# Kernel optimization log

Hardware: AMD Instinct MI355X
Metric: run time of the kernel (lower is better)

Reference implementation:

```python
import jax, jax.numpy as jnp
import numpy as np

NEG = -9e15  # sentinel used by the torch module for masked logits


def setup_inputs() -> dict:
    key = jax.random.key(0)
    k_x, k_nl, k_q, k_k, k_v = jax.random.split(key, 5)
    n, m, nhid = 50000, 16, 128
    x = jax.random.normal(k_x, (n, nhid), dtype=jnp.float32)
    neighbor_list = jax.random.randint(k_nl, (n, m), 0, n)  # value n-1 == padding
    # xavier_uniform with gain=1.414 for square (nhid, nhid) matrices
    bound = 1.414 * np.sqrt(6.0 / (nhid + nhid))
    Q = jax.random.uniform(k_q, (nhid, nhid), jnp.float32, -bound, bound)
    K = jax.random.uniform(k_k, (nhid, nhid), jnp.float32, -bound, bound)
    V = jax.random.uniform(k_v, (nhid, nhid), jnp.float32, -bound, bound)
    return {"x": x, "neighbor_list": neighbor_list, "Q": Q, "K": K, "V": V}


def _forward(x, neighbor_list, Q, K, V):
    n, nhid = x.shape
    scare = jnp.asarray(nhid ** 0.5, x.dtype)
    # masks: neighbor index n-1 means padding
    mask = (neighbor_list != n - 1).astype(x.dtype)            # (n, m)
    mask1 = mask[:, :, None] * mask[:, None, :]                # (n, m, m)
    mask2 = jnp.concatenate([jnp.ones((n, 1), x.dtype), mask], axis=1)[:, None, :]  # (n,1,m+1)

    # ---- stage 1: neighbor-level attention ----
    nm = x[neighbor_list]                                      # (n, m, h) gather
    Qn = jnp.einsum('nmk,kh->nmh', nm, Q)
    Kn = jnp.einsum('nmk,kh->nmh', nm, K)
    Vn = jnp.einsum('nmk,kh->nmh', nm, V)
    s = jnp.einsum('nih,njh->nij', Qn, Kn)                     # (n, m, m)
    s = jax.nn.leaky_relu(s, 0.01)
    s = jnp.where(mask1 > 0, s, NEG) * scare                   # faithful: scale after mask
    a = jax.nn.softmax(s, axis=2)                              # dropout is identity (eval)
    nres = jnp.einsum('nij,njh->nih', a, Vn)                   # (n, m, h)

    # ---- stage 2: node-level attention over [self, neighbors] ----
    xr = x[:, None, :]                                         # (n, 1, h)
    cat = jnp.concatenate([xr, nres], axis=1)                  # (n, m+1, h)
    Qx = jnp.einsum('nik,kh->nih', xr, Q)                      # (n, 1, h)
    Kc = jnp.einsum('njk,kh->njh', cat, K)
    Vc = jnp.einsum('njk,kh->njh', cat, V)
    s2 = jnp.einsum('nih,njh->nij', Qx, Kc) * scare            # (n, 1, m+1)
    s2 = jax.nn.leaky_relu(s2, 0.01)
    s2 = jnp.where(mask2 > 0, s2, NEG)
    a2 = jax.nn.softmax(s2, axis=2)
    out = jnp.einsum('nij,njh->nih', a2, Vc)[:, 0, :]          # (n, h)

    # F.normalize: L2 along dim 1, eps 1e-12
    norm = jnp.linalg.norm(out, axis=1, keepdims=True)
    return out / jnp.maximum(norm, 1e-12)


def reference(x, neighbor_list, Q, K, V):
    return _forward(x, neighbor_list, Q, K, V)
```

## Files before the change

kernel.cpp:

```cpp
#include <hip/hip_runtime.h>
#include <math.h>

#define NEG_CONST (-9000000000000000.0f)
#define SCARE 11.313708498984761f

#define DPP_XOR1  0xB1
#define DPP_XOR2  0x4E
#define DPP_XOR7  0x141
#define DPP_XOR15 0x140

template<int CTRL>
__device__ __forceinline__ float dpp_add(float x) {
    int yi = __builtin_amdgcn_update_dpp(0, __float_as_int(x), CTRL, 0xF, 0xF, true);
    return x + __int_as_float(yi);
}
template<int CTRL>
__device__ __forceinline__ float dpp_max(float x) {
    int yi = __builtin_amdgcn_update_dpp(0, __float_as_int(x), CTRL, 0xF, 0xF, true);
    return fmaxf(x, __int_as_float(yi));
}

__device__ __forceinline__ void wave_lds_fence() {
    __builtin_amdgcn_wave_barrier();
    asm volatile("s_waitcnt lgkmcnt(0)" ::: "memory");
    __builtin_amdgcn_wave_barrier();
}
__device__ __forceinline__ void wave_vm_fence() {
    __builtin_amdgcn_wave_barrier();
    asm volatile("s_waitcnt vmcnt(0) lgkmcnt(0)" ::: "memory");
    __builtin_amdgcn_wave_barrier();
}

__global__ __launch_bounds__(256) void small_mm_a(const float* __restrict__ Q,
                                                  const float* __restrict__ K,
                                                  const float* __restrict__ V,
                                                  float* __restrict__ QKt,
                                                  float* __restrict__ VV) {
    int r  = blockIdx.x * 8 + (threadIdx.x >> 5);
    int c0 = (threadIdx.x & 31) * 4;
    float a0 = 0.f, a1 = 0.f, a2 = 0.f, a3 = 0.f;
    if (blockIdx.y == 0) {
        for (int k = 0; k < 128; k += 4) {
            float4 q  = *reinterpret_cast<const float4*>(&Q[r * 128 + k]);
            float4 k0 = *reinterpret_cast<const float4*>(&K[(c0 + 0) * 128 + k]);
            float4 k1 = *reinterpret_cast<const float4*>(&K[(c0 + 1) * 128 + k]);
            float4 k2 = *reinterpret_cast<const float4*>(&K[(c0 + 2) * 128 + k]);
            float4 k3 = *reinterpret_cast<const float4*>(&K[(c0 + 3) * 128 + k]);
            a0 += q.x*k0.x + q.y*k0.y + q.z*k0.z + q.w*k0.w;
            a1 += q.x*k1.x + q.y*k1.y + q.z*k1.z + q.w*k1.w;
            a2 += q.x*k2.x + q.y*k2.y + q.z*k2.z + q.w*k2.w;
            a3 += q.x*k3.x + q.y*k3.y + q.z*k3.z + q.w*k3.w;
        }
        float4 o = {a0, a1, a2, a3};
        *reinterpret_cast<float4*>(&QKt[r * 128 + c0]) = o;
    } else {
        for (int k = 0; k < 128; ++k) {
            float a = V[r * 128 + k];
            float4 b = *reinterpret_cast<const float4*>(&V[k * 128 + c0]);
            a0 += a * b.x; a1 += a * b.y; a2 += a * b.z; a3 += a * b.w;
        }
        float4 o = {a0, a1, a2, a3};
        *reinterpret_cast<float4*>(&VV[r * 128 + c0]) = o;
    }
}

__global__ __launch_bounds__(256) void small_mm_b(const float* __restrict__ QKt,
                                                  const float* __restrict__ V,
                                                  float* __restrict__ MT) {
    int r  = blockIdx.x * 8 + (threadIdx.x >> 5);
    int c0 = (threadIdx.x & 31) * 4;
    float a0 = 0.f, a1 = 0.f, a2 = 0.f, a3 = 0.f;
    for (int k = 0; k < 128; k += 4) {
        float4 q  = *reinterpret_cast<const float4*>(&QKt[r * 128 + k]);
        float4 k0 = *reinterpret_cast<const float4*>(&V[(c0 + 0) * 128 + k]);
        float4 k1 = *reinterpret_cast<const float4*>(&V[(c0 + 1) * 128 + k]);
        float4 k2 = *reinterpret_cast<const float4*>(&V[(c0 + 2) * 128 + k]);
        float4 k3 = *reinterpret_cast<const float4*>(&V[(c0 + 3) * 128 + k]);
        a0 += q.x*k0.x + q.y*k0.y + q.z*k0.z + q.w*k0.w;
        a1 += q.x*k1.x + q.y*k1.y + q.z*k1.z + q.w*k1.w;
        a2 += q.x*k2.x + q.y*k2.y + q.z*k2.z + q.w*k2.w;
        a3 += q.x*k3.x + q.y*k3.y + q.z*k3.z + q.w*k3.w;
    }
    float4 o = {a0, a1, a2, a3};
    *reinterpret_cast<float4*>(&MT[r * 128 + c0]) = o;
}

__global__ __launch_bounds__(256) void proj_gemm(
    const float* __restrict__ x,
    const float* __restrict__ W0, const float* __restrict__ W1,
    const float* __restrict__ W2, const float* __restrict__ W3,
    float* __restrict__ O0, float* __restrict__ O1,
    float* __restrict__ O2, float* __restrict__ O3, int n)
{
    __shared__ __align__(16) float xs[32][132];
    __shared__ __align__(16) float ws[32][132];

    const float* Wsel[4] = {W0, W1, W2, W3};
    float*       Osel[4] = {O0, O1, O2, O3};
    const float* W = Wsel[blockIdx.y];
    float*       O = Osel[blockIdx.y];
    int row0 = blockIdx.x * 128;
    int tid = threadIdx.x;
    int tr = tid >> 4, tc = tid & 15;

    float acc[8][8] = {};
    for (int kk = 0; kk < 128; kk += 32) {
        #pragma unroll
        for (int it = 0; it < 4; ++it) {
            int id = tid + it * 256;
            int r = id >> 3;
            int f = id & 7;
            int grow = row0 + r;
            float4 v = (grow < n)
                ? *reinterpret_cast<const float4*>(&x[(size_t)grow * 128 + kk + f * 4])
                : make_float4(0.f, 0.f, 0.f, 0.f);
            xs[f * 4 + 0][r] = v.x; xs[f * 4 + 1][r] = v.y;
            xs[f * 4 + 2][r] = v.z; xs[f * 4 + 3][r] = v.w;
        }
        #pragma unroll
        for (int it = 0; it < 4; ++it) {
            int id = tid + it * 256;
            int k = id >> 5;
            int c4 = id & 31;
            *reinterpret_cast<float4*>(&ws[k][c4 * 4]) =
                *reinterpret_cast<const float4*>(&W[(size_t)(kk + k) * 128 + c4 * 4]);
        }
        __syncthreads();
        #pragma unroll 4
        for (int k = 0; k < 32; ++k) {
            float4 a0 = *reinterpret_cast<const float4*>(&xs[k][tr * 8]);
            float4 a1 = *reinterpret_cast<const float4*>(&xs[k][tr * 8 + 4]);
            float4 b0 = *reinterpret_cast<const float4*>(&ws[k][tc * 8]);
            float4 b1 = *reinterpret_cast<const float4*>(&ws[k][tc * 8 + 4]);
            float av[8] = {a0.x, a0.y, a0.z, a0.w, a1.x, a1.y, a1.z, a1.w};
            float bv[8] = {b0.x, b0.y, b0.z, b0.w, b1.x, b1.y, b1.z, b1.w};
            #pragma unroll
            for (int i2 = 0; i2 < 8; ++i2)
                #pragma unroll
                for (int j2 = 0; j2 < 8; ++j2)
                    acc[i2][j2] += av[i2] * bv[j2];
        }
        __syncthreads();
    }
    #pragma unroll
    for (int i2 = 0; i2 < 8; ++i2) {
        int grow = row0 + tr * 8 + i2;
        if (grow < n) {
            float4 o0 = {acc[i2][0], acc[i2][1], acc[i2][2], acc[i2][3]};
            float4 o1 = {acc[i2][4], acc[i2][5], acc[i2][6], acc[i2][7]};
            *reinterpret_cast<float4*>(&O[(size_t)grow * 128 + tc * 8])     = o0;
            *reinterpret_cast<float4*>(&O[(size_t)grow * 128 + tc * 8 + 4]) = o1;
        }
    }
}

__global__ __launch_bounds__(64, 5) void node_attn(
    const int* __restrict__ nlist,
    const float* __restrict__ x,
    const float* __restrict__ xQK,
    const float* __restrict__ u,
    const float* __restrict__ xV,
    const float* __restrict__ xVV,
    float* __restrict__ outp, int n)
{
    __shared__ __align__(16) float Bs[2048];
    __shared__ __align__(16) int   NLs[16];
    __shared__ __align__(16) float Ts[16];

    const int l  = threadIdx.x;
    const int g  = l >> 2;
    const int jj = l & 3;
    const int i  = blockIdx.x;

    int nlv = 0;
    if (l < 16) {
        nlv = nlist[(size_t)i * 16 + l];
        NLs[l] = nlv;
    }
    unsigned long long mb = __ballot(l < 16 ? (nlv != n - 1) : 0);

    {
        int sub   = l & 31;
        int sigma = ((sub & 3) << 3) | (sub >> 2);
        int half  = l >> 5;
        #pragma unroll
        for (int p = 0; p < 8; ++p) {
            int nr = __shfl(nlv, 2 * p + half, 64);
            const float* src = &x[(size_t)nr * 128 + sigma * 4];
            __builtin_amdgcn_global_load_lds(
                (const __attribute__((address_space(1))) unsigned int*)src,
                (__attribute__((address_space(3))) unsigned int*)&Bs[p * 256],
                16, 0, 0);
        }
    }

    float2 qa = *reinterpret_cast<const float2*>(&xQK[(size_t)i * 128 + l * 2]);
    float2 xa = *reinterpret_cast<const float2*>(&x[(size_t)i * 128 + l * 2]);
    float s200 = qa.x * xa.x + qa.y * xa.y;
    s200 = dpp_add<DPP_XOR1>(s200);
    s200 = dpp_add<DPP_XOR2>(s200);
    s200 = dpp_add<DPP_XOR7>(s200);
    s200 = dpp_add<DPP_XOR15>(s200);
    s200 += __shfl_xor(s200, 16, 64);
    s200 += __shfl_xor(s200, 32, 64);

    int nl_g = __shfl(nlv, g, 64);
    float4 A[8];
    {
        const float* ab = &xQK[(size_t)nl_g * 128 + jj * 32];
        #pragma unroll
        for (int k4 = 0; k4 < 8; ++k4)
            A[k4] = *reinterpret_cast<const float4*>(&ab[k4 * 4]);
    }

    wave_vm_fence();

    float a[16];
    {
        float sc[16];
        #pragma unroll
        for (int c = 0; c < 16; ++c) {
            const float* bb = &Bs[c * 128 + jj * 4];
            float acc = 0.f;
            #pragma unroll
            for (int k4 = 0; k4 < 8; ++k4) {
                float4 b = *reinterpret_cast<const float4*>(&bb[k4 * 16]);
                acc += A[k4].x * b.x + A[k4].y * b.y + A[k4].z * b.z + A[k4].w * b.w;
            }
            acc = dpp_add<DPP_XOR1>(acc);
            acc = dpp_add<DPP_XOR2>(acc);
            sc[c] = acc;
        }
        bool rlive = (mb >> g) & 1ULL;
        float m = -3.0e38f;
        #pragma unroll
        for (int c = 0; c < 16; ++c) {
            float s = sc[c];
            float slr = s > 0.f ? s : 0.01f * s;
            bool live = rlive && ((mb >> c) & 1ULL);
            float sm = (live ? slr : NEG_CONST) * SCARE;
            sc[c] = sm;
            m = fmaxf(m, sm);
        }
        float ssum = 0.f;
        #pragma unroll
        for (int c = 0; c < 16; ++c) { float p = __expf(sc[c] - m); a[c] = p; ssum += p; }
        float rs = 1.f / ssum;
        #pragma unroll
        for (int c = 0; c < 16; ++c) a[c] *= rs;
    }

    int nlarr[16];
    {
        int4 nlq[4];
        #pragma unroll
        for (int q4 = 0; q4 < 4; ++q4)
            nlq[q4] = *reinterpret_cast<const int4*>(&NLs[q4 * 4]);
        #pragma unroll
        for (int q4 = 0; q4 < 4; ++q4) {
            nlarr[q4 * 4 + 0] = nlq[q4].x; nlarr[q4 * 4 + 1] = nlq[q4].y;
            nlarr[q4 * 4 + 2] = nlq[q4].z; nlarr[q4 * 4 + 3] = nlq[q4].w;
        }
    }
    float2 vvreg[16];
    #pragma unroll
    for (int k = 0; k < 16; ++k)
        vvreg[k] = *reinterpret_cast<const float2*>(&xVV[(size_t)nlarr[k] * 128 + l * 2]);

    {
        float acc = 0.f;
        #pragma unroll
        for (int k4 = 0; k4 < 8; ++k4) {
            int kx = (k4 + g) & 7;
            float4 b  = *reinterpret_cast<const float4*>(&Bs[g * 128 + kx * 16 + jj * 4]);
            float4 uu = *reinterpret_cast<const float4*>(&u[(size_t)i * 128 + jj * 32 + kx * 4]);
            acc += uu.x * b.x + uu.y * b.y + uu.z * b.z + uu.w * b.w;
        }
        acc = dpp_add<DPP_XOR1>(acc);
        acc = dpp_add<DPP_XOR2>(acc);
        if (jj == 0) Ts[g] = acc;
    }
    wave_lds_fence();
    float tarr[16];
    {
        #pragma unroll
        for (int q4 = 0; q4 < 4; ++q4) {
            float4 t4 = *reinterpret_cast<const float4*>(&Ts[q4 * 4]);
            tarr[q4 * 4 + 0] = t4.x; tarr[q4 * 4 + 1] = t4.y;
            tarr[q4 * 4 + 2] = t4.z; tarr[q4 * 4 + 3] = t4.w;
        }
    }

    float lg = 0.f;
    #pragma unroll
    for (int k = 0; k < 16; ++k) lg += a[k] * tarr[k];
    {
        float v = lg * SCARE;
        v = v > 0.f ? v : 0.01f * v;
        lg = ((mb >> g) & 1ULL) ? v : NEG_CONST;
    }
    float v0 = s200 * SCARE;
    v0 = v0 > 0.f ? v0 : 0.01f * v0;

    float m17 = lg;
    m17 = dpp_max<DPP_XOR7>(m17);
    m17 = dpp_max<DPP_XOR15>(m17);
    m17 = fmaxf(m17, __shfl_xor(m17, 16, 64));
    m17 = fmaxf(m17, __shfl_xor(m17, 32, 64));
    m17 = fmaxf(m17, v0);
    float pg = __expf(lg - m17);
    float sg = pg;
    sg = dpp_add<DPP_XOR7>(sg);
    sg = dpp_add<DPP_XOR15>(sg);
    sg += __shfl_xor(sg, 16, 64);
    sg += __shfl_xor(sg, 32, 64);
    float p0 = __expf(v0 - m17);
    float inv = 1.f / (sg + p0);
    float a2g = pg * inv;
    float a20 = p0 * inv;

    float w[16];
    #pragma unroll
    for (int k = 0; k < 16; ++k) {
        float wv = a2g * a[k];
        wv = dpp_add<DPP_XOR7>(wv);
        wv = dpp_add<DPP_XOR15>(wv);
        wv += __shfl_xor(wv, 16, 64);
        wv += __shfl_xor(wv, 32, 64);
        w[k] = wv;
    }

    float2 xv = *reinterpret_cast<const float2*>(&xV[(size_t)i * 128 + l * 2]);
    float o0 = a20 * xv.x, o1 = a20 * xv.y;
    #pragma unroll
    for (int k = 0; k < 16; ++k) {
        o0 += w[k] * vvreg[k].x;
        o1 += w[k] * vvreg[k].y;
    }
    float sq = o0 * o0 + o1 * o1;
    sq = dpp_add<DPP_XOR1>(sq);
    sq = dpp_add<DPP_XOR2>(sq);
    sq = dpp_add<DPP_XOR7>(sq);
    sq = dpp_add<DPP_XOR15>(sq);
    sq += __shfl_xor(sq, 16, 64);
    sq += __shfl_xor(sq, 32, 64);
    float d = fmaxf(sqrtf(sq), 1e-12f);
    float rd = 1.f / d;
    float2 o = {o0 * rd, o1 * rd};
    *reinterpret_cast<float2*>(&outp[(size_t)i * 128 + l * 2]) = o;
}

extern "C" void kernel_launch(void* const* d_in, const int* in_sizes, int n_in,
                              void* d_out, int out_size, void* d_ws, size_t ws_size,
                              hipStream_t stream) {
    const float* x     = (const float*)d_in[0];
    const int*   nlist = (const int*)d_in[1];
    const float* Q     = (const float*)d_in[2];
    const float* K     = (const float*)d_in[3];
    const float* V     = (const float*)d_in[4];
    float* out = (float*)d_out;
    int n = in_sizes[0] / 128;

    float* ws   = (float*)d_ws;
    float* QKt  = ws;
    float* MT   = ws + 16384;
    float* VV   = ws + 32768;
    float* xQK  = ws + 49152;
    size_t stride = (size_t)n * 128;
    float* uarr = xQK + stride;
    float* xV   = uarr + stride;
    float* xVV  = xV + stride;

    small_mm_a<<<dim3(16, 2), 256, 0, stream>>>(Q, K, V, QKt, VV);
    small_mm_b<<<dim3(16), 256, 0, stream>>>(QKt, V, MT);
    dim3 g2((n + 127) / 128, 4);
    proj_gemm<<<g2, 256, 0, stream>>>(x, QKt, MT, V, VV, xQK, uarr, xV, xVV, n);
    node_attn<<<n, 64, 0, stream>>>(nlist, x, xQK, uarr, xV, xVV, out, n);
}
```

Measured before the change: 319.3 us.

## Replace xVV gather with per-node VV matvec and interleave x with xQK

Drops the precomputed xVV projection. Instead, node_attn forms the attention-weighted sum of the gathered neighbor x rows already in LDS, then multiplies it by the 128x128 VV matrix inside the kernel. This removes one GEMM output pass and 16 random neighbor row gathers per node. The GEMM also writes x and xQK interleaved into a 256-wide buffer G so each neighbor's rows share locality. In exchange, each node block does a 128x128 matvec with VV reads served from cache, plus an extra LDS round trip.

```diff
diff --git a/kernel.cpp b/kernel.cpp
--- a/kernel.cpp
+++ b/kernel.cpp
@@ -88,17 +88,22 @@
 __global__ __launch_bounds__(256) void proj_gemm(
     const float* __restrict__ x,
     const float* __restrict__ W0, const float* __restrict__ W1,
-    const float* __restrict__ W2, const float* __restrict__ W3,
-    float* __restrict__ O0, float* __restrict__ O1,
-    float* __restrict__ O2, float* __restrict__ O3, int n)
+    const float* __restrict__ W2,
+    float* __restrict__ G, float* __restrict__ O1, float* __restrict__ O2,
+    int n)
 {
     __shared__ __align__(16) float xs[32][132];
     __shared__ __align__(16) float ws[32][132];
 
-    const float* Wsel[4] = {W0, W1, W2, W3};
-    float*       Osel[4] = {O0, O1, O2, O3};
-    const float* W = Wsel[blockIdx.y];
-    float*       O = Osel[blockIdx.y];
+    const float* Wsel[3] = {W0, W1, W2};
+    float*       Osel[3] = {G, O1, O2};
+    const int    osr[3]  = {256, 128, 128};
+    const int    oof[3]  = {128, 0, 0};
+    int yb = blockIdx.y;
+    const float* W = Wsel[yb];
+    float*       O = Osel[yb];
+    int ostride = osr[yb];
+    int ooff = oof[yb];
     int row0 = blockIdx.x * 128;
     int tid = threadIdx.x;
     int tr = tid >> 4, tc = tid & 15;
@@ -116,6 +121,8 @@
                 : make_float4(0.f, 0.f, 0.f, 0.f);
             xs[f * 4 + 0][r] = v.x; xs[f * 4 + 1][r] = v.y;
             xs[f * 4 + 2][r] = v.z; xs[f * 4 + 3][r] = v.w;
+            if (yb == 0 && grow < n)
+                *reinterpret_cast<float4*>(&G[(size_t)grow * 256 + kk + f * 4]) = v;
         }
         #pragma unroll
         for (int it = 0; it < 4; ++it) {
@@ -148,24 +155,23 @@
         if (grow < n) {
             float4 o0 = {acc[i2][0], acc[i2][1], acc[i2][2], acc[i2][3]};
             float4 o1 = {acc[i2][4], acc[i2][5], acc[i2][6], acc[i2][7]};
-            *reinterpret_cast<float4*>(&O[(size_t)grow * 128 + tc * 8])     = o0;
-            *reinterpret_cast<float4*>(&O[(size_t)grow * 128 + tc * 8 + 4]) = o1;
+            *reinterpret_cast<float4*>(&O[(size_t)grow * ostride + ooff + tc * 8])     = o0;
+            *reinterpret_cast<float4*>(&O[(size_t)grow * ostride + ooff + tc * 8 + 4]) = o1;
         }
     }
 }
 
 __global__ __launch_bounds__(64, 5) void node_attn(
     const int* __restrict__ nlist,
-    const float* __restrict__ x,
-    const float* __restrict__ xQK,
+    const float* __restrict__ G,
     const float* __restrict__ u,
     const float* __restrict__ xV,
-    const float* __restrict__ xVV,
+    const float* __restrict__ VVm,
     float* __restrict__ outp, int n)
 {
     __shared__ __align__(16) float Bs[2048];
-    __shared__ __align__(16) int   NLs[16];
     __shared__ __align__(16) float Ts[16];
+    __shared__ __align__(16) float Ys[128];
 
     const int l  = threadIdx.x;
     const int g  = l >> 2;
@@ -173,10 +179,7 @@
     const int i  = blockIdx.x;
 
     int nlv = 0;
-    if (l < 16) {
-        nlv = nlist[(size_t)i * 16 + l];
-        NLs[l] = nlv;
-    }
+    if (l < 16) nlv = nlist[(size_t)i * 16 + l];
     unsigned long long mb = __ballot(l < 16 ? (nlv != n - 1) : 0);
 
     {
@@ -186,7 +189,7 @@
         #pragma unroll
         for (int p = 0; p < 8; ++p) {
             int nr = __shfl(nlv, 2 * p + half, 64);
-            const float* src = &x[(size_t)nr * 128 + sigma * 4];
+            const float* src = &G[(size_t)nr * 256 + sigma * 4];
             __builtin_amdgcn_global_load_lds(
                 (const __attribute__((address_space(1))) unsigned int*)src,
                 (__attribute__((address_space(3))) unsigned int*)&Bs[p * 256],
@@ -194,8 +197,8 @@
         }
     }
 
-    float2 qa = *reinterpret_cast<const float2*>(&xQK[(size_t)i * 128 + l * 2]);
-    float2 xa = *reinterpret_cast<const float2*>(&x[(size_t)i * 128 + l * 2]);
+    float2 qa = *reinterpret_cast<const float2*>(&G[(size_t)i * 256 + 128 + l * 2]);
+    float2 xa = *reinterpret_cast<const float2*>(&G[(size_t)i * 256 + l * 2]);
     float s200 = qa.x * xa.x + qa.y * xa.y;
     s200 = dpp_add<DPP_XOR1>(s200);
     s200 = dpp_add<DPP_XOR2>(s200);
@@ -207,7 +210,7 @@
     int nl_g = __shfl(nlv, g, 64);
     float4 A[8];
     {
-        const float* ab = &xQK[(size_t)nl_g * 128 + jj * 32];
+        const float* ab = &G[(size_t)nl_g * 256 + 128 + jj * 32];
         #pragma unroll
         for (int k4 = 0; k4 < 8; ++k4)
             A[k4] = *reinterpret_cast<const float4*>(&ab[k4 * 4]);
@@ -249,23 +252,6 @@
         #pragma unroll
         for (int c = 0; c < 16; ++c) a[c] *= rs;
     }
-
-    int nlarr[16];
-    {
-        int4 nlq[4];
-        #pragma unroll
-        for (int q4 = 0; q4 < 4; ++q4)
-            nlq[q4] = *reinterpret_cast<const int4*>(&NLs[q4 * 4]);
-        #pragma unroll
-        for (int q4 = 0; q4 < 4; ++q4) {
-            nlarr[q4 * 4 + 0] = nlq[q4].x; nlarr[q4 * 4 + 1] = nlq[q4].y;
-            nlarr[q4 * 4 + 2] = nlq[q4].z; nlarr[q4 * 4 + 3] = nlq[q4].w;
-        }
-    }
-    float2 vvreg[16];
-    #pragma unroll
-    for (int k = 0; k < 16; ++k)
-        vvreg[k] = *reinterpret_cast<const float2*>(&xVV[(size_t)nlarr[k] * 128 + l * 2]);
 
     {
         float acc = 0.f;
@@ -330,13 +316,56 @@
         w[k] = wv;
     }
 
+    {
+        int sg2 = l >> 1;
+        int tau = ((sg2 & 7) << 2) | (sg2 >> 3);
+        int off2 = (2 * l) & 3;
+        float y0 = 0.f, y1 = 0.f;
+        #pragma unroll
+        for (int k = 0; k < 16; ++k) {
+            const float* bp = &Bs[k * 128 + tau * 4 + off2];
+            y0 += w[k] * bp[0];
+            y1 += w[k] * bp[1];
+        }
+        float2 ywr = {y0, y1};
+        *reinterpret_cast<float2*>(&Ys[2 * l]) = ywr;
+    }
+    wave_lds_fence();
+
+    float p8[8] = {};
+    {
+        float4 ys[8];
+        #pragma unroll
+        for (int q = 0; q < 8; ++q)
+            ys[q] = *reinterpret_cast<const float4*>(&Ys[jj * 32 + q * 4]);
+        #pragma unroll
+        for (int q = 0; q < 8; ++q) {
+            float yv[4] = {ys[q].x, ys[q].y, ys[q].z, ys[q].w};
+            #pragma unroll
+            for (int e = 0; e < 4; ++e) {
+                int kidx = jj * 32 + q * 4 + e;
+                const float* row = &VVm[kidx * 128 + 8 * g];
+                float4 va = *reinterpret_cast<const float4*>(row);
+                float4 vb = *reinterpret_cast<const float4*>(row + 4);
+                float yk = yv[e];
+                p8[0] += yk * va.x; p8[1] += yk * va.y;
+                p8[2] += yk * va.z; p8[3] += yk * va.w;
+                p8[4] += yk * vb.x; p8[5] += yk * vb.y;
+                p8[6] += yk * vb.z; p8[7] += yk * vb.w;
+            }
+        }
+        #pragma unroll
+        for (int m = 0; m < 8; ++m) {
+            p8[m] = dpp_add<DPP_XOR1>(p8[m]);
+            p8[m] = dpp_add<DPP_XOR2>(p8[m]);
+        }
+    }
+    float gp0 = (jj == 0) ? p8[0] : (jj == 1) ? p8[2] : (jj == 2) ? p8[4] : p8[6];
+    float gp1 = (jj == 0) ? p8[1] : (jj == 1) ? p8[3] : (jj == 2) ? p8[5] : p8[7];
+
     float2 xv = *reinterpret_cast<const float2*>(&xV[(size_t)i * 128 + l * 2]);
-    float o0 = a20 * xv.x, o1 = a20 * xv.y;
-    #pragma unroll
-    for (int k = 0; k < 16; ++k) {
-        o0 += w[k] * vvreg[k].x;
-        o1 += w[k] * vvreg[k].y;
-    }
+    float o0 = a20 * xv.x + gp0;
+    float o1 = a20 * xv.y + gp1;
     float sq = o0 * o0 + o1 * o1;
     sq = dpp_add<DPP_XOR1>(sq);
     sq = dpp_add<DPP_XOR2>(sq);
@@ -365,15 +394,13 @@
     float* QKt  = ws;
     float* MT   = ws + 16384;
     float* VV   = ws + 32768;
-    float* xQK  = ws + 49152;
-    size_t stride = (size_t)n * 128;
-    float* uarr = xQK + stride;
-    float* xV   = uarr + stride;
-    float* xVV  = xV + stride;
+    float* G    = ws + 49152;
+    float* uarr = G + (size_t)n * 256;
+    float* xV   = uarr + (size_t)n * 128;
 
     small_mm_a<<<dim3(16, 2), 256, 0, stream>>>(Q, K, V, QKt, VV);
     small_mm_b<<<dim3(16), 256, 0, stream>>>(QKt, V, MT);
-    dim3 g2((n + 127) / 128, 4);
-    proj_gemm<<<g2, 256, 0, stream>>>(x, QKt, MT, V, VV, xQK, uarr, xV, xVV, n);
-    node_attn<<<n, 64, 0, stream>>>(nlist, x, xQK, uarr, xV, xVV, out, n);
-}
+    dim3 g2((n + 127) / 128, 3);
+    proj_gemm<<<g2, 256, 0, stream>>>(x, QKt, MT, V, G, uarr, xV, n);
+    node_attn<<<n, 64, 0, stream>>>(nlist, G, uarr, xV, VV, out, n);
+}
```

New measurement: 594.7 us. +86.3%, slower.
